# Kernel tuning notes

Measured on AMD Instinct MI355X. Metric: run time of the kernel, lower is better.

The kernel has to match this reference:

```python
import jax, jax.numpy as jnp
import numpy as np

N = 100000   # nodes
E = 1600000  # edges (avg degree 16)
D = 128      # feature dim (layer_sizes = [128, 128, 128])


def setup_inputs() -> dict:
    key = jax.random.key(0)
    ks = jax.random.split(key, 8)
    s = 1.0 / np.sqrt(D)  # glorot-ish scale for linear weights
    return {
        "x": jax.random.normal(ks[0], (N, D), jnp.float32),
        "edge_index": jax.random.randint(ks[1], (2, E), 0, N, dtype=jnp.int32),
        "perturb_first": jax.random.normal(ks[2], (N, D), jnp.float32) * 0.01,
        "perturb_last": jax.random.normal(ks[3], (N, D), jnp.float32) * 0.01,
        "W1": jax.random.normal(ks[4], (D, D), jnp.float32) * s,
        "b1": jnp.zeros((D,), jnp.float32),
        "W2": jax.random.normal(ks[5], (D, D), jnp.float32) * s,
        "b2": jnp.zeros((D,), jnp.float32),
    }


def reference(x, edge_index, perturb_first, perturb_last, W1, b1, W2, b2):
    n = x.shape[0]
    # PyG GCNConv: add self-loops, symmetric deg^{-1/2} normalization.
    loop = jnp.arange(n, dtype=edge_index.dtype)
    src = jnp.concatenate([edge_index[0], loop])  # [E+N]
    dst = jnp.concatenate([edge_index[1], loop])  # [E+N]
    deg = jax.ops.segment_sum(jnp.ones(dst.shape[0], x.dtype), dst, num_segments=n)
    dinv = jnp.where(deg > 0, 1.0 / jnp.sqrt(deg), 0.0)
    norm = (dinv[src] * dinv[dst])[:, None]  # [E+N, 1]

    def gcn_conv(h, W, b):
        h = h @ W.T                                   # linear (bias-free), [N, D]
        msg = h[src] * norm                           # gather + scale, [E+N, D]
        out = jax.ops.segment_sum(msg, dst, num_segments=n)  # scatter-add
        return out + b

    # forward only runs model[0] and model[3] (the two GCNConv layers);
    # norms and PReLU are skipped by the original forward.
    h = gcn_conv(x, W1, b1) + perturb_first
    out = gcn_conv(h, W2, b2) + perturb_last
    return out
```

## Files before the change

### kernel.cpp

```cpp
#include <hip/hip_runtime.h>
#include <math.h>

#define D 128
#define WS_PAD 132

typedef short bf16x8 __attribute__((ext_vector_type(8)));
typedef float f32x4 __attribute__((ext_vector_type(4)));

__device__ __forceinline__ unsigned short f2bf(float f) {
  unsigned u = __float_as_uint(f);
  u += 0x7FFFu + ((u >> 16) & 1u);
  return (unsigned short)(u >> 16);
}


__global__ __launch_bounds__(256) void count_deg_kernel(const int* __restrict__ dst, int E,
                                                        int* __restrict__ deg,
                                                        const float* __restrict__ W2,
                                                        unsigned short* __restrict__ W2bf) {
  int nbe = (E + 255) >> 8;
  int b = blockIdx.x;
  if (b >= nbe) {
    if (W2bf != nullptr) {
      int t = (b - nbe) * 256 + threadIdx.x;
      #pragma unroll
      for (int q = 0; q < 2; ++q) {
        int idx = t + q * 2048;
        float4 w = ((const float4*)W2)[idx];
        ushort4 o;
        o.x = f2bf(w.x); o.y = f2bf(w.y); o.z = f2bf(w.z); o.w = f2bf(w.w);
        ((ushort4*)W2bf)[idx] = o;
      }
    }
    return;
  }
  int e = b * 256 + threadIdx.x;
  if (e < E) atomicAdd(&deg[dst[e]], 1);
}


__global__ __launch_bounds__(256) void scan_blocksum_kernel(const int* __restrict__ deg, int n,
                                                            int* __restrict__ blockSums) {
  __shared__ int sm[256];
  int t = threadIdx.x;
  int i = blockIdx.x * 256 + t;
  sm[t] = (i < n) ? deg[i] : 0;
  __syncthreads();
  for (int off = 128; off > 0; off >>= 1) {
    if (t < off) sm[t] += sm[t + off];
    __syncthreads();
  }
  if (t == 0) blockSums[blockIdx.x] = sm[0];
}

__global__ __launch_bounds__(512) void scan_top_kernel(int* __restrict__ blockSums, int nb) {
  __shared__ int sm[512];
  int t = threadIdx.x;
  int v = (t < nb) ? blockSums[t] : 0;
  sm[t] = v;
  __syncthreads();
  for (int off = 1; off < 512; off <<= 1) {
    int x = (t >= off) ? sm[t - off] : 0;
    __syncthreads();
    sm[t] += x;
    __syncthreads();
  }
  if (t < nb) blockSums[t] = sm[t] - v;
}

__global__ __launch_bounds__(256) void scan_write_kernel(const int* __restrict__ deg, int n,
                                                         const int* __restrict__ blockSums,
                                                         int* __restrict__ ptr,
                                                         float* __restrict__ dinv) {
  __shared__ int sm[256];
  int t = threadIdx.x;
  int i = blockIdx.x * 256 + t;
  int v = (i < n) ? deg[i] : 0;
  sm[t] = v;
  __syncthreads();
  for (int off = 1; off < 256; off <<= 1) {
    int x = (t >= off) ? sm[t - off] : 0;
    __syncthreads();
    sm[t] += x;
    __syncthreads();
  }
  if (i < n) {
    ptr[i] = blockSums[blockIdx.x] + sm[t] - v;
    dinv[i] = 1.0f / sqrtf((float)(v + 1));
  }
}


__device__ __forceinline__ void gemm_body(const float* __restrict__ X,
                                          const float* __restrict__ W,
                                          const float* __restrict__ dinv,
                                          unsigned short* __restrict__ H, int n,
                                          int bid, int nblocks,
                                          float* __restrict__ Ws, float* __restrict__ Xs) {
  const int tid = threadIdx.x;
  const int tx = tid & 31;
  const int ty = tid >> 5;
  const int ntiles = (n + 31) >> 5;

  for (int tile = bid; tile < ntiles; tile += nblocks) {
    const int row0 = tile << 5;
    const int rows_here = min(32, n - row0);
    __syncthreads();
    {
      const float4* Xg = (const float4*)(X + (size_t)row0 * D);
      int tmax = rows_here * 32;
      for (int t = tid; t < tmax; t += 256) ((float4*)Xs)[t] = Xg[t];
    }
    float acc[4][4] = {{0.f}};
    #pragma unroll
    for (int kt = 0; kt < 128; kt += 64) {
      __syncthreads();
      for (int t = tid; t < 2048; t += 256) {
        int j  = t >> 4;
        int k4 = (t & 15) << 2;
        float4 w = ((const float4*)W)[j * 32 + (kt >> 2) + (t & 15)];
        Ws[(k4 + 0) * WS_PAD + j] = w.x;
        Ws[(k4 + 1) * WS_PAD + j] = w.y;
        Ws[(k4 + 2) * WS_PAD + j] = w.z;
        Ws[(k4 + 3) * WS_PAD + j] = w.w;
      }
      __syncthreads();
      #pragma unroll 4
      for (int k = 0; k < 64; ++k) {
        float4 w = *(const float4*)&Ws[k * WS_PAD + (tx << 2)];
        #pragma unroll
        for (int r = 0; r < 4; ++r) {
          float xv = Xs[(ty + 8 * r) * 128 + (kt + k)];
          acc[r][0] += xv * w.x;
          acc[r][1] += xv * w.y;
          acc[r][2] += xv * w.z;
          acc[r][3] += xv * w.w;
        }
      }
    }
    #pragma unroll
    for (int r = 0; r < 4; ++r) {
      int row = row0 + ty + 8 * r;
      if (row < n) {
        float s = dinv[row];
        unsigned h0 = f2bf(s * acc[r][0]);
        unsigned h1 = f2bf(s * acc[r][1]);
        unsigned h2 = f2bf(s * acc[r][2]);
        unsigned h3 = f2bf(s * acc[r][3]);
        ((uint2*)(H + (size_t)row * D))[tx] = make_uint2(h0 | (h1 << 16), h2 | (h3 << 16));
      }
    }
  }
}


#define FUSED_GRID 2048

__global__ __launch_bounds__(256) void fused_fill_gemm_kernel(
    const int* __restrict__ src, const int* __restrict__ dst,
    int* __restrict__ ptr, int* __restrict__ csr, int E,
    const float* __restrict__ X, const float* __restrict__ W,
    const float* __restrict__ dinv, unsigned short* __restrict__ H, int n) {
  __shared__ float Ws[64 * WS_PAD];
  __shared__ float Xs[32 * 128];
  int sub = blockIdx.x & 7;
  if (sub < 2) {
    int fb = (blockIdx.x >> 3) * 2 + sub;
    int stride = 512 * 256;
    for (int e = fb * 256 + threadIdx.x; e < E; e += stride) {
      int d = dst[e];
      int pos = atomicAdd(&ptr[d], 1);
      csr[pos] = src[e];
    }
  } else {
    int gb = (blockIdx.x >> 3) * 6 + (sub - 2);
    gemm_body(X, W, dinv, H, n, gb, 1536, Ws, Xs);
  }
}

__global__ __launch_bounds__(256) void gemm128_kernel(const float* __restrict__ X,
                                                      const float* __restrict__ W,
                                                      const float* __restrict__ dinv,
                                                      unsigned short* __restrict__ H, int n) {
  __shared__ float Ws[64 * WS_PAD];
  __shared__ float Xs[32 * 128];
  gemm_body(X, W, dinv, H, n, blockIdx.x, gridDim.x, Ws, Xs);
}


__device__ __forceinline__ void gather_row(const int* __restrict__ csr,
                                           const int* __restrict__ rend,
                                           const unsigned* __restrict__ Hu,
                                           int i, int lane, float& ax, float& ay) {
  int start = (i == 0) ? 0 : rend[i - 1];
  int end = rend[i];
  unsigned v = Hu[(size_t)i * 64 + lane];
  ax = __uint_as_float(v << 16);
  ay = __uint_as_float(v & 0xFFFF0000u);
  int e = start;
  for (; e + 8 <= end; e += 8) {
    unsigned w0 = Hu[(size_t)csr[e + 0] * 64 + lane];
    unsigned w1 = Hu[(size_t)csr[e + 1] * 64 + lane];
    unsigned w2 = Hu[(size_t)csr[e + 2] * 64 + lane];
    unsigned w3 = Hu[(size_t)csr[e + 3] * 64 + lane];
    unsigned w4 = Hu[(size_t)csr[e + 4] * 64 + lane];
    unsigned w5 = Hu[(size_t)csr[e + 5] * 64 + lane];
    unsigned w6 = Hu[(size_t)csr[e + 6] * 64 + lane];
    unsigned w7 = Hu[(size_t)csr[e + 7] * 64 + lane];
    ax += __uint_as_float(w0 << 16) + __uint_as_float(w1 << 16) +
          __uint_as_float(w2 << 16) + __uint_as_float(w3 << 16) +
          __uint_as_float(w4 << 16) + __uint_as_float(w5 << 16) +
          __uint_as_float(w6 << 16) + __uint_as_float(w7 << 16);
    ay += __uint_as_float(w0 & 0xFFFF0000u) + __uint_as_float(w1 & 0xFFFF0000u) +
          __uint_as_float(w2 & 0xFFFF0000u) + __uint_as_float(w3 & 0xFFFF0000u) +
          __uint_as_float(w4 & 0xFFFF0000u) + __uint_as_float(w5 & 0xFFFF0000u) +
          __uint_as_float(w6 & 0xFFFF0000u) + __uint_as_float(w7 & 0xFFFF0000u);
  }
  for (; e < end; ++e) {
    unsigned w = Hu[(size_t)csr[e] * 64 + lane];
    ax += __uint_as_float(w << 16);
    ay += __uint_as_float(w & 0xFFFF0000u);
  }
}


__global__ __launch_bounds__(256, 8) void gather_kernel(const int* __restrict__ csr,
                                                        const int* __restrict__ rend,
                                                        const float* __restrict__ dinv,
                                                        const unsigned* __restrict__ Hu,
                                                        const float* __restrict__ bias,
                                                        const float* __restrict__ perturb,
                                                        float* __restrict__ out, int n) {
  int i = (blockIdx.x << 2) + (threadIdx.x >> 6);
  if (i >= n) return;
  int lane = threadIdx.x & 63;
  float ax, ay;
  gather_row(csr, rend, Hu, i, lane, ax, ay);
  float di = dinv[i];
  float2 p = ((const float2*)(perturb + (size_t)i * D))[lane];
  float2 o;
  o.x = bias[2 * lane + 0] + p.x + di * ax;
  o.y = bias[2 * lane + 1] + p.y + di * ay;
  ((float2*)(out + (size_t)i * D))[lane] = o;
}


#define GG_PITCH 136

__global__ __launch_bounds__(512, 8) void gather_gemm_kernel(
    const int* __restrict__ csr, const int* __restrict__ rend,
    const float* __restrict__ dinv, const unsigned* __restrict__ Hu,
    const float* __restrict__ bias, const float* __restrict__ perturb,
    const unsigned short* __restrict__ W2bf, unsigned short* __restrict__ H2, int n) {
  __shared__ unsigned short Ts[32 * GG_PITCH];
  const int tid = threadIdx.x;
  const int wv = tid >> 6;
  const int lane = tid & 63;
  const int base = blockIdx.x << 5;

  #pragma unroll
  for (int j = 0; j < 4; ++j) {
    int row = (wv << 2) + j;
    int i = base + row;
    if (i < n) {
      float ax, ay;
      gather_row(csr, rend, Hu, i, lane, ax, ay);
      float di = dinv[i];
      float2 p = ((const float2*)(perturb + (size_t)i * D))[lane];
      float ox = bias[2 * lane + 0] + p.x + di * ax;
      float oy = bias[2 * lane + 1] + p.y + di * ay;
      unsigned pack = (unsigned)f2bf(ox) | ((unsigned)f2bf(oy) << 16);
      *(unsigned*)&Ts[row * GG_PITCH + (lane << 1)] = pack;
    }
  }
  __syncthreads();

  const int mt = wv >> 2;
  const int nt0 = wv & 3;
  const int m = lane & 15;
  const int quad = lane >> 4;
  const unsigned short* Wrow0 = W2bf + (size_t)(nt0 * 16 + m) * 128;
  const unsigned short* Wrow1 = W2bf + (size_t)((nt0 + 4) * 16 + m) * 128;
  f32x4 acc0 = {0.f, 0.f, 0.f, 0.f};
  f32x4 acc1 = {0.f, 0.f, 0.f, 0.f};
  #pragma unroll
  for (int s = 0; s < 4; ++s) {
    int k = (s << 5) + (quad << 3);
    bf16x8 a  = *(const bf16x8*)&Ts[(mt * 16 + m) * GG_PITCH + k];
    bf16x8 b0 = *(const bf16x8*)&Wrow0[k];
    bf16x8 b1 = *(const bf16x8*)&Wrow1[k];
    acc0 = __builtin_amdgcn_mfma_f32_16x16x32_bf16(a, b0, acc0, 0, 0, 0);
    acc1 = __builtin_amdgcn_mfma_f32_16x16x32_bf16(a, b1, acc1, 0, 0, 0);
  }
  #pragma unroll
  for (int r = 0; r < 4; ++r) {
    int row = mt * 16 + (quad << 2) + r;
    int g = base + row;
    if (g < n) {
      float s = dinv[g];
      H2[(size_t)g * D + nt0 * 16 + m]       = f2bf(s * acc0[r]);
      H2[(size_t)g * D + (nt0 + 4) * 16 + m] = f2bf(s * acc1[r]);
    }
  }
}


extern "C" void kernel_launch(void* const* d_in, const int* in_sizes, int n_in,
                              void* d_out, int out_size, void* d_ws, size_t ws_size,
                              hipStream_t stream) {
  const float* x  = (const float*)d_in[0];
  const int*   ei = (const int*)d_in[1];
  const float* pf = (const float*)d_in[2];
  const float* pl = (const float*)d_in[3];
  const float* W1 = (const float*)d_in[4];
  const float* b1 = (const float*)d_in[5];
  const float* W2 = (const float*)d_in[6];
  const float* b2 = (const float*)d_in[7];
  float* out = (float*)d_out;

  const int n = in_sizes[0] / D;
  const int E = in_sizes[1] / 2;
  const int* src = ei;
  const int* dst = ei + E;

  int*   deg       = (int*)d_ws;
  float* dinv      = (float*)d_ws + n;
  int*   ptr       = (int*)d_ws + 2 * n;
  int*   blockSums = (int*)d_ws + 3 * n;
  int*   csr       = (int*)d_ws + 3 * n + 512;
  size_t a1_off = ((size_t)(3 * n + 512 + E) * 4 + 255) & ~(size_t)255;
  unsigned short* A1 = (unsigned short*)((char*)d_ws + a1_off);
  unsigned short* A2 = A1 + (size_t)n * D;
  unsigned short* W2bf = A2 + (size_t)n * D;
  size_t needed = a1_off + (2 * (size_t)n * D + 128 * 128) * sizeof(unsigned short);
  const bool fused_l2 = (ws_size >= needed);

  const int nb_n = (n + 255) / 256;
  const int nb_e = (E + 255) / 256;
  const int nb_g = (n + 3) / 4;

  hipMemsetAsync(deg, 0, (size_t)n * sizeof(int), stream);
  count_deg_kernel<<<nb_e + 8, 256, 0, stream>>>(dst, E, deg, W2,
                                                 fused_l2 ? W2bf : (unsigned short*)nullptr);
  scan_blocksum_kernel<<<nb_n, 256, 0, stream>>>(deg, n, blockSums);
  scan_top_kernel<<<1, 512, 0, stream>>>(blockSums, nb_n);
  scan_write_kernel<<<nb_n, 256, 0, stream>>>(deg, n, blockSums, ptr, dinv);

  fused_fill_gemm_kernel<<<FUSED_GRID, 256, 0, stream>>>(src, dst, ptr, csr, E, x, W1, dinv, A1, n);

  if (fused_l2) {
    gather_gemm_kernel<<<(n + 31) / 32, 512, 0, stream>>>(csr, ptr, dinv, (const unsigned*)A1,
                                                          b1, pf, W2bf, A2, n);
    gather_kernel<<<nb_g, 256, 0, stream>>>(csr, ptr, dinv, (const unsigned*)A2, b2, pl, out, n);
  } else {
    gather_kernel<<<nb_g, 256, 0, stream>>>(csr, ptr, dinv, (const unsigned*)A1, b1, pf, out, n);
    gemm128_kernel<<<1024, 256, 0, stream>>>(out, W2, dinv, A1, n);
    gather_kernel<<<nb_g, 256, 0, stream>>>(csr, ptr, dinv, (const unsigned*)A1, b2, pl, out, n);
  }
}
```

Measured before the change: 569.1 us.

## Replace layer-1 FP32 GEMM with split-bf16 MFMA in fused CSR fill kernel

Layer-1 X@W1^T now runs on bf16 MFMA instructions using a hi/lo split of X and W1 (three MFMAs per product) to keep accuracy close to fp32, replacing the scalar fp32 shared-memory GEMM. W1 is pre-split into bf16 hi/lo halves by extra blocks in the degree-count kernel. The fused kernel also rebalances its work so half the blocks do the CSR fill and half do the GEMM, instead of a quarter and three quarters. The cost is three MFMAs per product plus on-the-fly conversion of X, and H is written with scattered 2-byte stores.

```diff
diff --git a/kernel.cpp b/kernel.cpp
--- a/kernel.cpp
+++ b/kernel.cpp
@@ -13,16 +13,25 @@
   return (unsigned short)(u >> 16);
 }
 
+__device__ __forceinline__ float bf2f(unsigned short h) {
+  return __uint_as_float(((unsigned)h) << 16);
+}
+
 
 __global__ __launch_bounds__(256) void count_deg_kernel(const int* __restrict__ dst, int E,
                                                         int* __restrict__ deg,
                                                         const float* __restrict__ W2,
-                                                        unsigned short* __restrict__ W2bf) {
+                                                        unsigned short* __restrict__ W2bf,
+                                                        const float* __restrict__ W1,
+                                                        unsigned short* __restrict__ W1h,
+                                                        unsigned short* __restrict__ W1l) {
   int nbe = (E + 255) >> 8;
   int b = blockIdx.x;
   if (b >= nbe) {
-    if (W2bf != nullptr) {
-      int t = (b - nbe) * 256 + threadIdx.x;
+    if (W2bf == nullptr) return;
+    int which = b - nbe;
+    if (which < 8) {
+      int t = which * 256 + threadIdx.x;
       #pragma unroll
       for (int q = 0; q < 2; ++q) {
         int idx = t + q * 2048;
@@ -30,6 +39,20 @@
         ushort4 o;
         o.x = f2bf(w.x); o.y = f2bf(w.y); o.z = f2bf(w.z); o.w = f2bf(w.w);
         ((ushort4*)W2bf)[idx] = o;
+      }
+    } else {
+      int t = (which - 8) * 256 + threadIdx.x;
+      #pragma unroll
+      for (int q = 0; q < 2; ++q) {
+        int idx = t + q * 2048;
+        float4 w = ((const float4*)W1)[idx];
+        ushort4 hi, lo;
+        hi.x = f2bf(w.x); lo.x = f2bf(w.x - bf2f(hi.x));
+        hi.y = f2bf(w.y); lo.y = f2bf(w.y - bf2f(hi.y));
+        hi.z = f2bf(w.z); lo.z = f2bf(w.z - bf2f(hi.z));
+        hi.w = f2bf(w.w); lo.w = f2bf(w.w - bf2f(hi.w));
+        ((ushort4*)W1h)[idx] = hi;
+        ((ushort4*)W1l)[idx] = lo;
       }
     }
     return;
@@ -153,8 +176,6 @@
   }
 }
 
-
-#define FUSED_GRID 2048
 
 __global__ __launch_bounds__(256) void fused_fill_gemm_kernel(
     const int* __restrict__ src, const int* __restrict__ dst,
@@ -185,6 +206,105 @@
   __shared__ float Ws[64 * WS_PAD];
   __shared__ float Xs[32 * 128];
   gemm_body(X, W, dinv, H, n, blockIdx.x, gridDim.x, Ws, Xs);
+}
+
+
+#define FUSED_GRID 2048
+#define G1_PITCH 136
+
+__global__ __launch_bounds__(256) void fused_fill_mfma_kernel(
+    const int* __restrict__ src, const int* __restrict__ dst,
+    int* __restrict__ ptr, int* __restrict__ csr, int E,
+    const float* __restrict__ X,
+    const unsigned short* __restrict__ W1h, const unsigned short* __restrict__ W1l,
+    const float* __restrict__ dinv, unsigned short* __restrict__ H, int n) {
+  __shared__ unsigned short Ths[32 * G1_PITCH];
+  __shared__ unsigned short Tls[32 * G1_PITCH];
+  int sub = blockIdx.x & 7;
+  if (sub < 4) {
+    int fb = (blockIdx.x >> 3) * 4 + sub;
+    int stride = 1024 * 256;
+    for (int e = fb * 256 + threadIdx.x; e < E; e += stride) {
+      int d = dst[e];
+      int pos = atomicAdd(&ptr[d], 1);
+      csr[pos] = src[e];
+    }
+  } else {
+    int gb = (blockIdx.x >> 3) * 4 + (sub - 4);
+    const int tid = threadIdx.x;
+    const int wv = tid >> 6;
+    const int lane = tid & 63;
+    const int m = lane & 15;
+    const int quad = lane >> 4;
+    const int mt = wv >> 1;
+    const int ntb = (wv & 1) * 4;
+    const int ntiles = (n + 31) >> 5;
+
+    for (int tile = gb; tile < ntiles; tile += 1024) {
+      const int row0 = tile << 5;
+      const int rows_here = min(32, n - row0);
+      __syncthreads();
+      {
+        const float4* Xg = (const float4*)(X + (size_t)row0 * D);
+        int tmax = rows_here * 32;
+        for (int t = tid; t < tmax; t += 256) {
+          float4 xv = Xg[t];
+          int r = t >> 5, c4 = (t & 31) << 2;
+          ushort4 hi, lo;
+          hi.x = f2bf(xv.x); lo.x = f2bf(xv.x - bf2f(hi.x));
+          hi.y = f2bf(xv.y); lo.y = f2bf(xv.y - bf2f(hi.y));
+          hi.z = f2bf(xv.z); lo.z = f2bf(xv.z - bf2f(hi.z));
+          hi.w = f2bf(xv.w); lo.w = f2bf(xv.w - bf2f(hi.w));
+          *(ushort4*)&Ths[r * G1_PITCH + c4] = hi;
+          *(ushort4*)&Tls[r * G1_PITCH + c4] = lo;
+        }
+      }
+      __syncthreads();
+
+      f32x4 acc0 = {0.f, 0.f, 0.f, 0.f};
+      f32x4 acc1 = {0.f, 0.f, 0.f, 0.f};
+      f32x4 acc2 = {0.f, 0.f, 0.f, 0.f};
+      f32x4 acc3 = {0.f, 0.f, 0.f, 0.f};
+      #pragma unroll
+      for (int s = 0; s < 4; ++s) {
+        int k = (s << 5) + (quad << 3);
+        bf16x8 ah = *(const bf16x8*)&Ths[(mt * 16 + m) * G1_PITCH + k];
+        bf16x8 al = *(const bf16x8*)&Tls[(mt * 16 + m) * G1_PITCH + k];
+        bf16x8 bh0 = *(const bf16x8*)&W1h[(size_t)((ntb + 0) * 16 + m) * 128 + k];
+        bf16x8 bl0 = *(const bf16x8*)&W1l[(size_t)((ntb + 0) * 16 + m) * 128 + k];
+        acc0 = __builtin_amdgcn_mfma_f32_16x16x32_bf16(ah, bh0, acc0, 0, 0, 0);
+        acc0 = __builtin_amdgcn_mfma_f32_16x16x32_bf16(al, bh0, acc0, 0, 0, 0);
+        acc0 = __builtin_amdgcn_mfma_f32_16x16x32_bf16(ah, bl0, acc0, 0, 0, 0);
+        bf16x8 bh1 = *(const bf16x8*)&W1h[(size_t)((ntb + 1) * 16 + m) * 128 + k];
+        bf16x8 bl1 = *(const bf16x8*)&W1l[(size_t)((ntb + 1) * 16 + m) * 128 + k];
+        acc1 = __builtin_amdgcn_mfma_f32_16x16x32_bf16(ah, bh1, acc1, 0, 0, 0);
+        acc1 = __builtin_amdgcn_mfma_f32_16x16x32_bf16(al, bh1, acc1, 0, 0, 0);
+        acc1 = __builtin_amdgcn_mfma_f32_16x16x32_bf16(ah, bl1, acc1, 0, 0, 0);
+        bf16x8 bh2 = *(const bf16x8*)&W1h[(size_t)((ntb + 2) * 16 + m) * 128 + k];
+        bf16x8 bl2 = *(const bf16x8*)&W1l[(size_t)((ntb + 2) * 16 + m) * 128 + k];
+        acc2 = __builtin_amdgcn_mfma_f32_16x16x32_bf16(ah, bh2, acc2, 0, 0, 0);
+        acc2 = __builtin_amdgcn_mfma_f32_16x16x32_bf16(al, bh2, acc2, 0, 0, 0);
+        acc2 = __builtin_amdgcn_mfma_f32_16x16x32_bf16(ah, bl2, acc2, 0, 0, 0);
+        bf16x8 bh3 = *(const bf16x8*)&W1h[(size_t)((ntb + 3) * 16 + m) * 128 + k];
+        bf16x8 bl3 = *(const bf16x8*)&W1l[(size_t)((ntb + 3) * 16 + m) * 128 + k];
+        acc3 = __builtin_amdgcn_mfma_f32_16x16x32_bf16(ah, bh3, acc3, 0, 0, 0);
+        acc3 = __builtin_amdgcn_mfma_f32_16x16x32_bf16(al, bh3, acc3, 0, 0, 0);
+        acc3 = __builtin_amdgcn_mfma_f32_16x16x32_bf16(ah, bl3, acc3, 0, 0, 0);
+      }
+      #pragma unroll
+      for (int r = 0; r < 4; ++r) {
+        int row = mt * 16 + (quad << 2) + r;
+        int g = row0 + row;
+        if (g < n) {
+          float sc = dinv[g];
+          H[(size_t)g * D + (ntb + 0) * 16 + m] = f2bf(sc * acc0[r]);
+          H[(size_t)g * D + (ntb + 1) * 16 + m] = f2bf(sc * acc1[r]);
+          H[(size_t)g * D + (ntb + 2) * 16 + m] = f2bf(sc * acc2[r]);
+          H[(size_t)g * D + (ntb + 3) * 16 + m] = f2bf(sc * acc3[r]);
+        }
+      }
+    }
+  }
 }
 
 
@@ -332,7 +452,9 @@
   unsigned short* A1 = (unsigned short*)((char*)d_ws + a1_off);
   unsigned short* A2 = A1 + (size_t)n * D;
   unsigned short* W2bf = A2 + (size_t)n * D;
-  size_t needed = a1_off + (2 * (size_t)n * D + 128 * 128) * sizeof(unsigned short);
+  unsigned short* W1h  = W2bf + 128 * 128;
+  unsigned short* W1l  = W1h + 128 * 128;
+  size_t needed = a1_off + (2 * (size_t)n * D + 3 * 128 * 128) * sizeof(unsigned short);
   const bool fused_l2 = (ws_size >= needed);
 
   const int nb_n = (n + 255) / 256;
@@ -340,19 +462,20 @@
   const int nb_g = (n + 3) / 4;
 
   hipMemsetAsync(deg, 0, (size_t)n * sizeof(int), stream);
-  count_deg_kernel<<<nb_e + 8, 256, 0, stream>>>(dst, E, deg, W2,
-                                                 fused_l2 ? W2bf : (unsigned short*)nullptr);
+  count_deg_kernel<<<nb_e + 16, 256, 0, stream>>>(
+      dst, E, deg, W2, fused_l2 ? W2bf : (unsigned short*)nullptr, W1, W1h, W1l);
   scan_blocksum_kernel<<<nb_n, 256, 0, stream>>>(deg, n, blockSums);
   scan_top_kernel<<<1, 512, 0, stream>>>(blockSums, nb_n);
   scan_write_kernel<<<nb_n, 256, 0, stream>>>(deg, n, blockSums, ptr, dinv);
 
-  fused_fill_gemm_kernel<<<FUSED_GRID, 256, 0, stream>>>(src, dst, ptr, csr, E, x, W1, dinv, A1, n);
-
   if (fused_l2) {
+    fused_fill_mfma_kernel<<<FUSED_GRID, 256, 0, stream>>>(src, dst, ptr, csr, E, x, W1h, W1l,
+                                                           dinv, A1, n);
     gather_gemm_kernel<<<(n + 31) / 32, 512, 0, stream>>>(csr, ptr, dinv, (const unsigned*)A1,
                                                           b1, pf, W2bf, A2, n);
     gather_kernel<<<nb_g, 256, 0, stream>>>(csr, ptr, dinv, (const unsigned*)A2, b2, pl, out, n);
   } else {
+    fused_fill_gemm_kernel<<<FUSED_GRID, 256, 0, stream>>>(src, dst, ptr, csr, E, x, W1, dinv, A1, n);
     gather_kernel<<<nb_g, 256, 0, stream>>>(csr, ptr, dinv, (const unsigned*)A1, b1, pf, out, n);
     gemm128_kernel<<<1024, 256, 0, stream>>>(out, W2, dinv, A1, n);
     gather_kernel<<<nb_g, 256, 0, stream>>>(csr, ptr, dinv, (const unsigned*)A1, b2, pl, out, n);
```

New measurement: 564.7 us. No clear change (-0.8%).
